# Kernel optimization log

Hardware: AMD Instinct MI355X
Metric: run time of the kernel (lower is better)

Reference implementation:

```python
import jax, jax.numpy as jnp
import numpy as np

V, E, B, T, F, H, WIN, PAD = 50000, 64, 64, 1024, 128, 128, 3, 1


def setup_inputs() -> dict:
    key = jax.random.key(0)
    ks = jax.random.split(key, 14)
    s = 0.05
    ipts = jax.random.randint(ks[0], (B, T), 0, V, dtype=jnp.int32)
    seq_lengths = jax.random.randint(ks[1], (B,), T // 4, T + 1, dtype=jnp.int32)
    hidden = jnp.zeros((2, B, H), jnp.float32)  # (2*nlayers, B, H) bidirectional init state
    emb = (jax.random.normal(ks[2], (V, E), jnp.float32) * s).at[0].set(0.0)  # padding_idx=0
    conv_w = jax.random.normal(ks[3], (F, 1, WIN, E), jnp.float32) * s
    conv_b = jnp.zeros((F,), jnp.float32)
    w_ih_f = jax.random.normal(ks[4], (3 * H, F), jnp.float32) * s
    w_hh_f = jax.random.normal(ks[5], (3 * H, H), jnp.float32) * s
    b_ih_f = jnp.zeros((3 * H,), jnp.float32)
    b_hh_f = jnp.zeros((3 * H,), jnp.float32)
    w_ih_b = jax.random.normal(ks[6], (3 * H, F), jnp.float32) * s
    w_hh_b = jax.random.normal(ks[7], (3 * H, H), jnp.float32) * s
    b_ih_b = jnp.zeros((3 * H,), jnp.float32)
    b_hh_b = jnp.zeros((3 * H,), jnp.float32)
    lin_w = jax.random.normal(ks[8], (1, 2 * H), jnp.float32) * s
    lin_b = jnp.zeros((1,), jnp.float32)
    return dict(ipts=ipts, seq_lengths=seq_lengths, hidden=hidden, emb=emb,
                conv_w=conv_w, conv_b=conv_b,
                w_ih_f=w_ih_f, w_hh_f=w_hh_f, b_ih_f=b_ih_f, b_hh_f=b_hh_f,
                w_ih_b=w_ih_b, w_hh_b=w_hh_b, b_ih_b=b_ih_b, b_hh_b=b_hh_b,
                lin_w=lin_w, lin_b=lin_b)


def _gru(x_tbf, h0, w_ih, w_hh, b_ih, b_hh):
    # PyTorch GRU equations; input gate projections precomputed for all steps.
    xp = jnp.einsum('tbf,gf->tbg', x_tbf, w_ih) + b_ih  # (T,B,3H)

    def step(h, xp_t):
        gh = h @ w_hh.T + b_hh
        xr, xz, xn = jnp.split(xp_t, 3, axis=-1)
        hr, hz, hn = jnp.split(gh, 3, axis=-1)
        r = jax.nn.sigmoid(xr + hr)
        z = jax.nn.sigmoid(xz + hz)
        n = jnp.tanh(xn + r * hn)
        h_new = (1.0 - z) * n + z * h
        return h_new, h_new

    _, out = jax.lax.scan(step, h0, xp)
    return out  # (T,B,H)


def reference(ipts, seq_lengths, hidden, emb, conv_w, conv_b,
              w_ih_f, w_hh_f, b_ih_f, b_hh_f,
              w_ih_b, w_hh_b, b_ih_b, b_hh_b, lin_w, lin_b):
    x = emb[ipts]                                   # (B,T,E)
    c = jax.lax.conv_general_dilated(
        x[:, None, :, :], conv_w, (1, 1), [(PAD, PAD), (0, 0)],
        dimension_numbers=('NCHW', 'OIHW', 'NCHW'))    # (B,F,T,1)
    feats = jnp.transpose(c[..., 0] + conv_b[None, :, None], (0, 2, 1))  # (B,T,F)

    lens = seq_lengths
    t = jnp.arange(T)
    mask = (t[None, :] < lens[:, None]).astype(feats.dtype)             # (B,T)

    # forward direction over padded seq (pad positions masked out of the mean)
    out_f = _gru(jnp.transpose(feats, (1, 0, 2)), hidden[0], w_ih_f, w_hh_f, b_ih_f, b_hh_f)
    # backward direction: packed-sequence semantics -> reverse within the valid length
    rev_idx = jnp.clip(lens[:, None] - 1 - t[None, :], 0, T - 1)        # (B,T)
    feats_rev = jnp.take_along_axis(feats, rev_idx[:, :, None], axis=1)
    out_b = _gru(jnp.transpose(feats_rev, (1, 0, 2)), hidden[1], w_ih_b, w_hh_b, b_ih_b, b_hh_b)

    # masked mean over time (fused segment reduce replacing the python loop)
    m_tb = mask.T[:, :, None]                        # (T,B,1)
    denom = lens.astype(feats.dtype)[:, None]        # (B,1)
    mot_f = (out_f * m_tb).sum(0) / denom            # (B,H)
    mot_b = (out_b * m_tb).sum(0) / denom            # (B,H)
    mot = jnp.concatenate([mot_f, mot_b], axis=-1)   # (B,2H)

    out = jax.nn.sigmoid(mot @ lin_w.T + lin_b)      # (B,1)
    return out.squeeze()
```

## Files before the change

### kernel.cpp

```cpp
#include <hip/hip_runtime.h>


typedef __attribute__((ext_vector_type(8))) unsigned short ushort8;
typedef __attribute__((ext_vector_type(8))) short bf16x8;
typedef __attribute__((ext_vector_type(4))) float f32x4;

__device__ __forceinline__ unsigned short f2bf(float f) {
  unsigned int u = __float_as_uint(f);
  u += 0x7fffu + ((u >> 16) & 1u);
  return (unsigned short)(u >> 16);
}
__device__ __forceinline__ float bf2f(unsigned short us) {
  return __uint_as_float(((unsigned int)us) << 16);
}
#if __has_builtin(__builtin_amdgcn_sdot4)
#define SDOT4(a, b, c) __builtin_amdgcn_sdot4((int)(a), (int)(b), (c), false)
#else
__device__ __forceinline__ int sdot4_sw(int a, int b, int c) {
#pragma unroll
  for (int i = 0; i < 4; ++i)
    c += ((a << (24 - 8 * i)) >> 24) * ((b << (24 - 8 * i)) >> 24);
  return c;
}
#define SDOT4(a, b, c) sdot4_sw((int)(a), (int)(b), (c))
#endif
#define DPP_X1(x) __builtin_amdgcn_update_dpp(0, (x), 0xB1, 0xF, 0xF, true)

__global__ void k0_fuse(const float* __restrict__ conv_w, const float* __restrict__ conv_b,
                        const float* __restrict__ w_ih_f, const float* __restrict__ b_ih_f,
                        const float* __restrict__ w_ih_b, const float* __restrict__ b_ih_b,
                        const float* __restrict__ b_hh_f, const float* __restrict__ b_hh_b,
                        unsigned short* __restrict__ CWb, float* __restrict__ xbias) {
  int flat = blockIdx.x * 256 + threadIdx.x;
  if (flat >= 768 * 192) return;
  int g = flat / 192, k = flat % 192;
  const float* wih = (g < 384) ? w_ih_f : w_ih_b;
  int gg = (g < 384) ? g : g - 384;
  float acc = 0.f;
  for (int f = 0; f < 128; ++f) acc += wih[gg * 128 + f] * conv_w[f * 192 + k];
  CWb[g * 192 + k] = f2bf(acc);
  if (k == 0) {
    const float* bih = (g < 384) ? b_ih_f : b_ih_b;
    const float* bhh = (g < 384) ? b_hh_f : b_hh_b;
    float bb = bih[gg];
    if (gg < 256) bb += bhh[gg];
    for (int f = 0; f < 128; ++f) bb += wih[gg * 128 + f] * conv_b[f];
    xbias[g] = bb;
  }
}

__global__ void k0b_quant(const float* __restrict__ w_hh_f, const float* __restrict__ w_hh_b,
                          unsigned int* __restrict__ Wq8, float* __restrict__ ws) {
  int tid = blockIdx.x * 256 + threadIdx.x;
  int R = tid >> 5, dw = tid & 31;
  if (R >= 768) return;
  int dir = R / 384, rr = R - dir * 384;
  const float* w = (dir ? w_hh_b : w_hh_f) + (size_t)rr * 128 + dw * 4;
  float4 v = *reinterpret_cast<const float4*>(w);
  float am = fmaxf(fmaxf(fabsf(v.x), fabsf(v.y)), fmaxf(fabsf(v.z), fabsf(v.w)));
#pragma unroll
  for (int m = 1; m < 32; m <<= 1) am = fmaxf(am, __shfl_xor(am, m));
  float inv = (am > 0.f) ? 127.f / am : 0.f;
  int q0 = (int)rintf(v.x * inv), q1 = (int)rintf(v.y * inv);
  int q2 = (int)rintf(v.z * inv), q3 = (int)rintf(v.w * inv);
  unsigned int pk = (q0 & 255) | ((q1 & 255) << 8) | ((q2 & 255) << 16) | ((q3 & 255) << 24);
  Wq8[R * 32 + dw] = pk;
  if (dw == 0) ws[R] = am / 16129.f;
}

__global__ __launch_bounds__(256) void k1_gemm(const int* __restrict__ ipts,
                                               const float* __restrict__ emb,
                                               const unsigned short* __restrict__ CWb,
                                               const float* __restrict__ xbias,
                                               unsigned short* __restrict__ xp) {
  __shared__ __align__(16) unsigned short xs[130][72];
  __shared__ __align__(16) unsigned short wsb[128][200];
  const int bid = blockIdx.x;
  const int gb = bid % 6, tb = bid / 6;
  const int b = tb >> 3, t0 = (tb & 7) << 7, g0 = gb << 7;
  const int tid = threadIdx.x;

  for (int c = tid; c < 130 * 16; c += 256) {
    int row = c >> 4, cc = c & 15;
    int t = t0 - 1 + row;
    float4 v = make_float4(0.f, 0.f, 0.f, 0.f);
    if (t >= 0 && t < 1024) {
      int tok = ipts[b * 1024 + t];
      v = *reinterpret_cast<const float4*>(emb + (size_t)tok * 64 + cc * 4);
    }
    ushort4 pv;
    pv.x = f2bf(v.x); pv.y = f2bf(v.y); pv.z = f2bf(v.z); pv.w = f2bf(v.w);
    *reinterpret_cast<ushort4*>(&xs[row][cc * 4]) = pv;
  }
  for (int c = tid; c < 128 * 24; c += 256) {
    int g = c / 24, cc = c % 24;
    *reinterpret_cast<ushort8*>(&wsb[g][cc * 8]) =
        *reinterpret_cast<const ushort8*>(CWb + (size_t)(g0 + g) * 192 + cc * 8);
  }
  __syncthreads();

  const int lane = tid & 63, wid = tid >> 6;
  const int wy = wid >> 1, wx = wid & 1;
  const int ln15 = lane & 15, lhi = lane >> 4;

  f32x4 acc[4][4];
#pragma unroll
  for (int i = 0; i < 4; ++i)
#pragma unroll
    for (int j = 0; j < 4; ++j) acc[i][j] = (f32x4){0.f, 0.f, 0.f, 0.f};

#pragma unroll
  for (int kk = 0; kk < 6; ++kk) {
    const int w = kk >> 1;
    const int e0 = (kk & 1) * 32 + lhi * 8;
    const int k0 = kk * 32 + lhi * 8;
    bf16x8 a[4], bb[4];
#pragma unroll
    for (int i = 0; i < 4; ++i)
      a[i] = *reinterpret_cast<const bf16x8*>(&xs[wy * 64 + i * 16 + ln15 + w][e0]);
#pragma unroll
    for (int j = 0; j < 4; ++j)
      bb[j] = *reinterpret_cast<const bf16x8*>(&wsb[wx * 64 + j * 16 + ln15][k0]);
#pragma unroll
    for (int i = 0; i < 4; ++i)
#pragma unroll
      for (int j = 0; j < 4; ++j)
        acc[i][j] = __builtin_amdgcn_mfma_f32_16x16x32_bf16(a[i], bb[j], acc[i][j], 0, 0, 0);
  }

  float bias[4];
#pragma unroll
  for (int j = 0; j < 4; ++j) bias[j] = xbias[g0 + wx * 64 + j * 16 + ln15];

  unsigned short* outp = xp + (size_t)(b * 1024 + t0 + wy * 64) * 768 + g0 + wx * 64;
#pragma unroll
  for (int i = 0; i < 4; ++i)
#pragma unroll
    for (int r = 0; r < 4; ++r) {
      int m = i * 16 + lhi * 4 + r;
#pragma unroll
      for (int j = 0; j < 4; ++j)
        outp[(size_t)m * 768 + j * 16 + ln15] = f2bf(acc[i][j][r] + bias[j]);
    }
}

__global__ __launch_bounds__(256, 1) void k2_scan(
    const int* __restrict__ seqlen, const float* __restrict__ hidden,
    const float* __restrict__ b_hh_f, const float* __restrict__ b_hh_b,
    const unsigned int* __restrict__ Wq8, const float* __restrict__ ws,
    const unsigned short* __restrict__ xp, float* __restrict__ mot) {
  __shared__ __align__(16) unsigned int hq[2][32];
  const int tid = threadIdx.x;
  const int b = blockIdx.x & 63, dir = blockIdx.x >> 6;
  const int row = tid >> 1;
  const int half = tid & 1;
  const float* bhh = dir ? b_hh_b : b_hh_f;

  uint4 Wq[3][4];
#pragma unroll
  for (int g = 0; g < 3; ++g) {
    const uint4* rp = reinterpret_cast<const uint4*>(
        Wq8 + (size_t)(dir * 384 + g * 128 + row) * 32 + half * 16);
#pragma unroll
    for (int c = 0; c < 4; ++c)
      asm volatile("global_load_dwordx4 %0, %1, off"
                   : "=v"(Wq[g][c]) : "v"(rp + c) : "memory");
  }
  asm volatile("s_waitcnt vmcnt(0)" ::: "memory");
  __builtin_amdgcn_sched_barrier(0);

  const float sc0 = ws[dir * 384 + row];
  const float sc1 = ws[dir * 384 + 128 + row];
  const float sc2 = ws[dir * 384 + 256 + row];
  const float bh2 = bhh[256 + row];

  const int len = seqlen[b];
  float h = hidden[(size_t)(dir * 64 + b) * 128 + row];
  float acc = 0.f;
  if (!half) {
    int q = (int)rintf(h * 127.f) & 255;
    reinterpret_cast<unsigned char*>(&hq[0][0])[row] = (unsigned char)q;
  }

  const unsigned short* xpb = xp + (size_t)b * (1024 * 768) + dir * 384 + row;
  unsigned int xa0, xa1, xa2, xb0, xb1, xb2;
  int row2;
  {
    const int r0 = dir ? (len - 1) : 0;
    const int r1 = dir ? (len - 2) : 1;
    const unsigned short* q0 = xpb + (size_t)r0 * 768;
    const unsigned short* q1 = xpb + (size_t)r1 * 768;
    asm volatile("global_load_ushort %0, %1, off"            : "=v"(xa0) : "v"(q0) : "memory");
    asm volatile("global_load_ushort %0, %1, off offset:256" : "=v"(xa1) : "v"(q0) : "memory");
    asm volatile("global_load_ushort %0, %1, off offset:512" : "=v"(xa2) : "v"(q0) : "memory");
    asm volatile("global_load_ushort %0, %1, off"            : "=v"(xb0) : "v"(q1) : "memory");
    asm volatile("global_load_ushort %0, %1, off offset:256" : "=v"(xb1) : "v"(q1) : "memory");
    asm volatile("global_load_ushort %0, %1, off offset:512" : "=v"(xb2) : "v"(q1) : "memory");
    row2 = dir ? (len - 3 >= 0 ? len - 3 : 0) : (2 < len ? 2 : len - 1);
  }
  asm volatile("s_waitcnt lgkmcnt(0)" ::: "memory");
  __builtin_amdgcn_s_barrier();
  __builtin_amdgcn_sched_barrier(0);

#define K2_STEP(T_, CUR_, X0_, X1_, X2_)                                              \
  {                                                                                   \
    asm volatile("s_waitcnt vmcnt(3)" ::: "memory");                                  \
    __builtin_amdgcn_sched_barrier(0);                                                \
    const float xr = bf2f((unsigned short)(X0_));                                     \
    const float xz = bf2f((unsigned short)(X1_));                                     \
    const float xn = bf2f((unsigned short)(X2_));                                     \
    {                                                                                 \
      const unsigned short* pp = xpb + (size_t)row2 * 768;                            \
      asm volatile("global_load_ushort %0, %1, off"            : "=v"(X0_) : "v"(pp) : "memory"); \
      asm volatile("global_load_ushort %0, %1, off offset:256" : "=v"(X1_) : "v"(pp) : "memory"); \
      asm volatile("global_load_ushort %0, %1, off offset:512" : "=v"(X2_) : "v"(pp) : "memory"); \
      row2 = dir ? (row2 > 0 ? row2 - 1 : 0) : (row2 + 1 < len ? row2 + 1 : len - 1); \
    }                                                                                 \
    int ar = 0, az = 0, an = 0;                                                       \
    _Pragma("unroll")                                                                 \
    for (int c = 0; c < 4; ++c) {                                                     \
      const uint4 hv = *reinterpret_cast<const uint4*>(&hq[CUR_][half * 16 + c * 4]); \
      ar = SDOT4(Wq[0][c].x, hv.x, ar); ar = SDOT4(Wq[0][c].y, hv.y, ar);             \
      ar = SDOT4(Wq[0][c].z, hv.z, ar); ar = SDOT4(Wq[0][c].w, hv.w, ar);             \
      az = SDOT4(Wq[1][c].x, hv.x, az); az = SDOT4(Wq[1][c].y, hv.y, az);             \
      az = SDOT4(Wq[1][c].z, hv.z, az); az = SDOT4(Wq[1][c].w, hv.w, az);             \
      an = SDOT4(Wq[2][c].x, hv.x, an); an = SDOT4(Wq[2][c].y, hv.y, an);             \
      an = SDOT4(Wq[2][c].z, hv.z, an); an = SDOT4(Wq[2][c].w, hv.w, an);             \
    }                                                                                 \
    ar += DPP_X1(ar); az += DPP_X1(az); an += DPP_X1(an);                             \
    const float rr = 1.f / (1.f + __expf(-(xr + sc0 * (float)ar)));                   \
    const float zz = 1.f / (1.f + __expf(-(xz + sc1 * (float)az)));                   \
    const float na = xn + rr * (sc2 * (float)an + bh2);                               \
    const float e2 = __expf(2.f * na);                                                \
    const float nn = (e2 - 1.f) / (e2 + 1.f);                                         \
    const float hnew = (1.f - zz) * nn + zz * h;                                      \
    if ((T_) < len) {                                                                 \
      h = hnew; acc += hnew;                                                          \
      if (!half) {                                                                    \
        int q = (int)rintf(hnew * 127.f) & 255;                                       \
        reinterpret_cast<unsigned char*>(&hq[(CUR_) ^ 1][0])[row] = (unsigned char)q; \
      }                                                                               \
    }                                                                                 \
    asm volatile("s_waitcnt lgkmcnt(0)" ::: "memory");                                \
    __builtin_amdgcn_s_barrier();                                                     \
    __builtin_amdgcn_sched_barrier(0);                                                \
  }

  const int len2 = (len + 1) & ~1;
  for (int t = 0; t < len2; t += 2) {
    K2_STEP(t, 0, xa0, xa1, xa2);
    K2_STEP(t + 1, 1, xb0, xb1, xb2);
  }
#undef K2_STEP

  if (!half) mot[(size_t)b * 256 + dir * 128 + row] = acc / (float)len;
}

__global__ void k3_final(const float* __restrict__ mot, const float* __restrict__ lin_w,
                         const float* __restrict__ lin_b, float* __restrict__ out) {
  int tid = threadIdx.x;
  int b = tid >> 2, part = tid & 3;
  float s = 0.f;
  for (int i = 0; i < 64; ++i) s += mot[b * 256 + part * 64 + i] * lin_w[part * 64 + i];
  s += __shfl_xor(s, 1);
  s += __shfl_xor(s, 2);
  if (part == 0) out[b] = 1.f / (1.f + __expf(-(s + lin_b[0])));
}

extern "C" void kernel_launch(void* const* d_in, const int* in_sizes, int n_in,
                              void* d_out, int out_size, void* d_ws, size_t ws_size,
                              hipStream_t stream) {
  const int*   ipts    = (const int*)d_in[0];
  const int*   seqlen  = (const int*)d_in[1];
  const float* hidden  = (const float*)d_in[2];
  const float* emb     = (const float*)d_in[3];
  const float* conv_w  = (const float*)d_in[4];
  const float* conv_b  = (const float*)d_in[5];
  const float* w_ih_f  = (const float*)d_in[6];
  const float* w_hh_f  = (const float*)d_in[7];
  const float* b_ih_f  = (const float*)d_in[8];
  const float* b_hh_f  = (const float*)d_in[9];
  const float* w_ih_b  = (const float*)d_in[10];
  const float* w_hh_b  = (const float*)d_in[11];
  const float* b_ih_b  = (const float*)d_in[12];
  const float* b_hh_b  = (const float*)d_in[13];
  const float* lin_w   = (const float*)d_in[14];
  const float* lin_b   = (const float*)d_in[15];

  char* ws_ = (char*)d_ws;
  unsigned short* CWb = (unsigned short*)(ws_);
  float* xbias = (float*)(ws_ + 294912);
  float* mot   = (float*)(ws_ + 298240);
  unsigned int* Wq8 = (unsigned int*)(ws_ + 363776);
  float* wsc   = (float*)(ws_ + 462080);
  unsigned short* xp = (unsigned short*)(ws_ + 1048576);
  float* out = (float*)d_out;

  hipLaunchKernelGGL(k0_fuse, dim3(576), dim3(256), 0, stream,
                     conv_w, conv_b, w_ih_f, b_ih_f, w_ih_b, b_ih_b, b_hh_f, b_hh_b,
                     CWb, xbias);
  hipLaunchKernelGGL(k0b_quant, dim3(96), dim3(256), 0, stream,
                     w_hh_f, w_hh_b, Wq8, wsc);
  hipLaunchKernelGGL(k1_gemm, dim3(3072), dim3(256), 0, stream,
                     ipts, emb, CWb, xbias, xp);
  hipLaunchKernelGGL(k2_scan, dim3(128), dim3(256), 0, stream,
                     seqlen, hidden, b_hh_f, b_hh_b, Wq8, wsc, xp, mot);
  hipLaunchKernelGGL(k3_final, dim3(1), dim3(256), 0, stream, mot, lin_w, lin_b, out);
}
```

Baseline: 483.4 us.

## Merge weight-prep kernels, stage GEMM output through LDS, fma-fuse GRU gates

Folds the recurrent-weight quantization kernel into the conv/input-weight fusion kernel by splitting on block index, which removes one launch. The GEMM kernel now writes its bf16 output tile into shared memory first, then stores it to global with 16-byte coalesced writes instead of scattered 2-byte stores. This needs one extra barrier per tile. The scan's gate arithmetic is rewritten with explicit fmaf calls to shorten the serial dependency chain in each recurrent step.

```diff
diff --git a/kernel.cpp b/kernel.cpp
--- a/kernel.cpp
+++ b/kernel.cpp
@@ -30,42 +30,45 @@
                         const float* __restrict__ w_ih_f, const float* __restrict__ b_ih_f,
                         const float* __restrict__ w_ih_b, const float* __restrict__ b_ih_b,
                         const float* __restrict__ b_hh_f, const float* __restrict__ b_hh_b,
-                        unsigned short* __restrict__ CWb, float* __restrict__ xbias) {
-  int flat = blockIdx.x * 256 + threadIdx.x;
-  if (flat >= 768 * 192) return;
-  int g = flat / 192, k = flat % 192;
-  const float* wih = (g < 384) ? w_ih_f : w_ih_b;
-  int gg = (g < 384) ? g : g - 384;
-  float acc = 0.f;
-  for (int f = 0; f < 128; ++f) acc += wih[gg * 128 + f] * conv_w[f * 192 + k];
-  CWb[g * 192 + k] = f2bf(acc);
-  if (k == 0) {
-    const float* bih = (g < 384) ? b_ih_f : b_ih_b;
-    const float* bhh = (g < 384) ? b_hh_f : b_hh_b;
-    float bb = bih[gg];
-    if (gg < 256) bb += bhh[gg];
-    for (int f = 0; f < 128; ++f) bb += wih[gg * 128 + f] * conv_b[f];
-    xbias[g] = bb;
-  }
-}
-
-__global__ void k0b_quant(const float* __restrict__ w_hh_f, const float* __restrict__ w_hh_b,
-                          unsigned int* __restrict__ Wq8, float* __restrict__ ws) {
-  int tid = blockIdx.x * 256 + threadIdx.x;
-  int R = tid >> 5, dw = tid & 31;
-  if (R >= 768) return;
-  int dir = R / 384, rr = R - dir * 384;
-  const float* w = (dir ? w_hh_b : w_hh_f) + (size_t)rr * 128 + dw * 4;
-  float4 v = *reinterpret_cast<const float4*>(w);
-  float am = fmaxf(fmaxf(fabsf(v.x), fabsf(v.y)), fmaxf(fabsf(v.z), fabsf(v.w)));
-#pragma unroll
-  for (int m = 1; m < 32; m <<= 1) am = fmaxf(am, __shfl_xor(am, m));
-  float inv = (am > 0.f) ? 127.f / am : 0.f;
-  int q0 = (int)rintf(v.x * inv), q1 = (int)rintf(v.y * inv);
-  int q2 = (int)rintf(v.z * inv), q3 = (int)rintf(v.w * inv);
-  unsigned int pk = (q0 & 255) | ((q1 & 255) << 8) | ((q2 & 255) << 16) | ((q3 & 255) << 24);
-  Wq8[R * 32 + dw] = pk;
-  if (dw == 0) ws[R] = am / 16129.f;
+                        const float* __restrict__ w_hh_f, const float* __restrict__ w_hh_b,
+                        unsigned short* __restrict__ CWb, float* __restrict__ xbias,
+                        unsigned int* __restrict__ Wq8, float* __restrict__ wsq) {
+  const int bid = blockIdx.x;
+  if (bid < 576) {
+    int flat = bid * 256 + threadIdx.x;
+    if (flat >= 768 * 192) return;
+    int g = flat / 192, k = flat % 192;
+    const float* wih = (g < 384) ? w_ih_f : w_ih_b;
+    int gg = (g < 384) ? g : g - 384;
+    float acc = 0.f;
+    for (int f = 0; f < 128; ++f) acc += wih[gg * 128 + f] * conv_w[f * 192 + k];
+    CWb[g * 192 + k] = f2bf(acc);
+    if (k == 0) {
+      const float* bih = (g < 384) ? b_ih_f : b_ih_b;
+      const float* bhh = (g < 384) ? b_hh_f : b_hh_b;
+      float bb = bih[gg];
+      if (gg < 256) bb += bhh[gg];
+      for (int f = 0; f < 128; ++f) bb += wih[gg * 128 + f] * conv_b[f];
+      xbias[g] = bb;
+    }
+  } else {
+    int tid = (bid - 576) * 256 + threadIdx.x;
+    int R = tid >> 5, dw = tid & 31;
+    if (R >= 768) return;
+    int dir = R / 384, rr = R - dir * 384;
+    const float* w = (dir ? w_hh_b : w_hh_f) + (size_t)rr * 128 + dw * 4;
+    float4 v = *reinterpret_cast<const float4*>(w);
+    float am = fmaxf(fmaxf(fabsf(v.x), fabsf(v.y)), fmaxf(fabsf(v.z), fabsf(v.w)));
+#pragma unroll
+    for (int m = 1; m < 32; m <<= 1) am = fmaxf(am, __shfl_xor(am, m));
+    float inv = (am > 0.f) ? 127.f / am : 0.f;
+    int q0 = (int)rintf(v.x * inv), q1 = (int)rintf(v.y * inv);
+    int q2 = (int)rintf(v.z * inv), q3 = (int)rintf(v.w * inv);
+    unsigned int pk =
+        (q0 & 255) | ((q1 & 255) << 8) | ((q2 & 255) << 16) | ((q3 & 255) << 24);
+    Wq8[R * 32 + dw] = pk;
+    if (dw == 0) wsq[R] = am / 16129.f;
+  }
 }
 
 __global__ __launch_bounds__(256) void k1_gemm(const int* __restrict__ ipts,
@@ -73,8 +76,9 @@
                                                const unsigned short* __restrict__ CWb,
                                                const float* __restrict__ xbias,
                                                unsigned short* __restrict__ xp) {
-  __shared__ __align__(16) unsigned short xs[130][72];
-  __shared__ __align__(16) unsigned short wsb[128][200];
+  __shared__ __align__(16) unsigned short smem[130 * 72 + 128 * 200];
+  unsigned short* xs = smem;
+  unsigned short* wsb = smem + 130 * 72;
   const int bid = blockIdx.x;
   const int gb = bid % 6, tb = bid / 6;
   const int b = tb >> 3, t0 = (tb & 7) << 7, g0 = gb << 7;
@@ -90,11 +94,11 @@
     }
     ushort4 pv;
     pv.x = f2bf(v.x); pv.y = f2bf(v.y); pv.z = f2bf(v.z); pv.w = f2bf(v.w);
-    *reinterpret_cast<ushort4*>(&xs[row][cc * 4]) = pv;
+    *reinterpret_cast<ushort4*>(&xs[row * 72 + cc * 4]) = pv;
   }
   for (int c = tid; c < 128 * 24; c += 256) {
     int g = c / 24, cc = c % 24;
-    *reinterpret_cast<ushort8*>(&wsb[g][cc * 8]) =
+    *reinterpret_cast<ushort8*>(&wsb[g * 200 + cc * 8]) =
         *reinterpret_cast<const ushort8*>(CWb + (size_t)(g0 + g) * 192 + cc * 8);
   }
   __syncthreads();
@@ -117,10 +121,10 @@
     bf16x8 a[4], bb[4];
 #pragma unroll
     for (int i = 0; i < 4; ++i)
-      a[i] = *reinterpret_cast<const bf16x8*>(&xs[wy * 64 + i * 16 + ln15 + w][e0]);
+      a[i] = *reinterpret_cast<const bf16x8*>(&xs[(wy * 64 + i * 16 + ln15 + w) * 72 + e0]);
 #pragma unroll
     for (int j = 0; j < 4; ++j)
-      bb[j] = *reinterpret_cast<const bf16x8*>(&wsb[wx * 64 + j * 16 + ln15][k0]);
+      bb[j] = *reinterpret_cast<const bf16x8*>(&wsb[(wx * 64 + j * 16 + ln15) * 200 + k0]);
 #pragma unroll
     for (int i = 0; i < 4; ++i)
 #pragma unroll
@@ -132,16 +136,27 @@
 #pragma unroll
   for (int j = 0; j < 4; ++j) bias[j] = xbias[g0 + wx * 64 + j * 16 + ln15];
 
-  unsigned short* outp = xp + (size_t)(b * 1024 + t0 + wy * 64) * 768 + g0 + wx * 64;
+  __syncthreads();
+  unsigned short* ct = smem;
 #pragma unroll
   for (int i = 0; i < 4; ++i)
 #pragma unroll
     for (int r = 0; r < 4; ++r) {
-      int m = i * 16 + lhi * 4 + r;
+      const int tt = wy * 64 + i * 16 + lhi * 4 + r;
 #pragma unroll
       for (int j = 0; j < 4; ++j)
-        outp[(size_t)m * 768 + j * 16 + ln15] = f2bf(acc[i][j][r] + bias[j]);
+        ct[tt * 136 + wx * 64 + j * 16 + ln15] = f2bf(acc[i][j][r] + bias[j]);
     }
+  __syncthreads();
+
+  const size_t base = (size_t)(b * 1024 + t0);
+#pragma unroll
+  for (int it = 0; it < 8; ++it) {
+    const int flat = it * 256 + tid;
+    const int tt = flat >> 4, c8 = flat & 15;
+    ushort8 v = *reinterpret_cast<const ushort8*>(&ct[tt * 136 + c8 * 8]);
+    *reinterpret_cast<ushort8*>(xp + (base + tt) * 768 + g0 + c8 * 8) = v;
+  }
 }
 
 __global__ __launch_bounds__(256, 1) void k2_scan(
@@ -228,12 +243,12 @@
       an = SDOT4(Wq[2][c].z, hv.z, an); an = SDOT4(Wq[2][c].w, hv.w, an);             \
     }                                                                                 \
     ar += DPP_X1(ar); az += DPP_X1(az); an += DPP_X1(an);                             \
-    const float rr = 1.f / (1.f + __expf(-(xr + sc0 * (float)ar)));                   \
-    const float zz = 1.f / (1.f + __expf(-(xz + sc1 * (float)az)));                   \
-    const float na = xn + rr * (sc2 * (float)an + bh2);                               \
+    const float rr = 1.f / (1.f + __expf(-fmaf(sc0, (float)ar, xr)));                 \
+    const float zz = 1.f / (1.f + __expf(-fmaf(sc1, (float)az, xz)));                 \
+    const float na = fmaf(rr, fmaf(sc2, (float)an, bh2), xn);                         \
     const float e2 = __expf(2.f * na);                                                \
     const float nn = (e2 - 1.f) / (e2 + 1.f);                                         \
-    const float hnew = (1.f - zz) * nn + zz * h;                                      \
+    const float hnew = fmaf(zz, h - nn, nn);                                          \
     if ((T_) < len) {                                                                 \
       h = hnew; acc += hnew;                                                          \
       if (!half) {                                                                    \
@@ -296,11 +311,9 @@
   unsigned short* xp = (unsigned short*)(ws_ + 1048576);
   float* out = (float*)d_out;
 
-  hipLaunchKernelGGL(k0_fuse, dim3(576), dim3(256), 0, stream,
+  hipLaunchKernelGGL(k0_fuse, dim3(672), dim3(256), 0, stream,
                      conv_w, conv_b, w_ih_f, b_ih_f, w_ih_b, b_ih_b, b_hh_f, b_hh_b,
-                     CWb, xbias);
-  hipLaunchKernelGGL(k0b_quant, dim3(96), dim3(256), 0, stream,
-                     w_hh_f, w_hh_b, Wq8, wsc);
+                     w_hh_f, w_hh_b, CWb, xbias, Wq8, wsc);
   hipLaunchKernelGGL(k1_gemm, dim3(3072), dim3(256), 0, stream,
                      ipts, emb, CWb, xbias, xp);
   hipLaunchKernelGGL(k2_scan, dim3(128), dim3(256), 0, stream,
```

After: 508.3 us. +5.2%, slower.
